# Kernel tuning notes

Hardware: AMD Instinct MI355X
Metric: run time of the kernel (lower is better)

## Reference

```python
import jax, jax.numpy as jnp
import numpy as np

N_STEPS = 8          # spatial_interval
SPATIAL_SCALE = 1.0  # spatial_scale


def setup_inputs() -> dict:
    key = jax.random.key(0)
    ks = jax.random.split(key, 6)
    B, N, D = 32, 1024, 256
    x = jax.random.normal(ks[0], (B, N, D), dtype=jnp.float32)
    adj_mx = jax.random.uniform(ks[1], (N, N), dtype=jnp.float32) / N  # row-scaled dense adjacency
    alpha_train = jnp.ones((N,), dtype=jnp.float32)          # alpha * ones(num_node), alpha=1.0
    w = jnp.eye(D, dtype=jnp.float32) + 0.01 * jax.random.normal(ks[2], (D, D), dtype=jnp.float32)
    d = jax.random.uniform(ks[3], (D,), dtype=jnp.float32)
    fc_in_w = jax.random.normal(ks[4], (D, D), dtype=jnp.float32) * (1.0 / np.sqrt(D))
    fc_in_b = jnp.zeros((D,), dtype=jnp.float32)
    return {"x": x, "adj_mx": adj_mx, "alpha_train": alpha_train, "w": w,
            "d": d, "fc_in_w": fc_in_w, "fc_in_b": fc_in_b, "vt": 0}


def reference(x, adj_mx, alpha_train, w, d, fc_in_w, fc_in_b, vt):
    # x: [B, N, D]. x0 is detached in torch (x.clone().detach()).
    x0 = jax.lax.stop_gradient(x)
    # fc_in (dropout is identity in eval mode)
    h = jnp.einsum('bnd,ed->bne', x, fc_in_w) + fc_in_b
    # constants of the diffusion ODE
    alph = jax.nn.sigmoid(alpha_train)[:, None]          # [N, 1]
    d_clamped = jnp.clip(d, 0.0, 1.0)
    w_eff = (w * d_clamped) @ w.T                        # [D, D]
    dt = jnp.float32(SPATIAL_SCALE / N_STEPS)

    def euler_step(h, _):
        ax = jnp.einsum('nm,bmd->bnd', adj_mx, h)        # graph diffusion
        f = alph * 0.5 * (ax - h) + h @ w_eff - h + x0
        return h + dt * f, None

    h, _ = jax.lax.scan(euler_step, h, None, length=N_STEPS)
    return h
```

## Files before the change

### kernel.cpp

```cpp
#include <hip/hip_runtime.h>
#include <hip/hip_bf16.h>
#include <stdint.h>

typedef __bf16 bf16;
typedef __bf16 bf16x8 __attribute__((ext_vector_type(8)));
typedef __bf16 bf16x4 __attribute__((ext_vector_type(4)));
typedef float f32x4 __attribute__((ext_vector_type(4)));
typedef unsigned short u16;

__device__ __forceinline__ void gload_lds16(const bf16* g, bf16* l) {
    __builtin_amdgcn_global_load_lds(
        (const __attribute__((address_space(1))) void*)g,
        (__attribute__((address_space(3))) void*)l, 16, 0, 0);
}

template <int LD>
__device__ __forceinline__ void stage(const bf16* __restrict__ g, bf16* l, int t) {
    int sw = ((t & 7) ^ ((t >> 3) & 7)) << 3;
    size_t base = (size_t)(t >> 3) * LD + sw;
#pragma unroll
    for (int k = 0; k < 4; ++k)
        gload_lds16(g + base + (size_t)(k * 32) * LD, l + t * 8 + k * 2048);
}

#define LDSW(buf, row, kc) \
    (*(const bf16x8*)&(buf)[(row) * 64 + ((((kc) ^ ((row) & 7))) << 3)])

__global__ void prep_alpha(const float* __restrict__ a, float* __restrict__ out) {
    int i = blockIdx.x * blockDim.x + threadIdx.x;
    if (i < 1024) out[i] = 0.5f / (1.0f + __expf(-a[i]));
}

__global__ void prep_adj(const float* __restrict__ adj, const float* __restrict__ ahs,
                         bf16* __restrict__ adjb) {
    int i = blockIdx.x * blockDim.x + threadIdx.x;
    int row = i >> 8;
    float s = ahs[row];
    float4 v = ((const float4*)adj)[i];
    bf16x4 o = {(bf16)(s * v.x), (bf16)(s * v.y), (bf16)(s * v.z), (bf16)(s * v.w)};
    ((bf16x4*)adjb)[i] = o;
}

__global__ void cast_f32_bf16x4(const float* __restrict__ src, bf16* __restrict__ dst,
                                int n4) {
    int i = blockIdx.x * blockDim.x + threadIdx.x;
    if (i < n4) {
        float4 v = ((const float4*)src)[i];
        bf16x4 o = {(bf16)v.x, (bf16)v.y, (bf16)v.z, (bf16)v.w};
        ((bf16x4*)dst)[i] = o;
    }
}

__global__ void prep_weff(const float* __restrict__ w, const float* __restrict__ dv,
                          bf16* __restrict__ weffT) {
    __shared__ float wk[256];
    __shared__ float dd[256];
    int k = blockIdx.x, j = threadIdx.x;
    dd[j] = fminf(fmaxf(dv[j], 0.0f), 1.0f);
    wk[j] = w[k * 256 + j];
    __syncthreads();
    float s = 0.0f;
#pragma unroll 8
    for (int c = 0; c < 256; ++c) s += wk[c] * dd[c] * w[j * 256 + c];
    weffT[j * 256 + k] = (bf16)s;
}

__global__ void prep_xT(const float* __restrict__ x, bf16* __restrict__ xT,
                        bf16* __restrict__ xb) {
    __shared__ bf16 tile[64][65];
    int b = blockIdx.z, n0 = blockIdx.x * 64, d0 = blockIdx.y * 64;
    int t = threadIdx.x;
    int i = t >> 4, j4 = (t & 15) * 4;
#pragma unroll
    for (int p = 0; p < 4; ++p) {
        int n = i + p * 16;
        size_t gi = (((size_t)b << 10) + n0 + n) * 256 + d0 + j4;
        float4 v = *(const float4*)&x[gi];
        bf16x4 o = {(bf16)v.x, (bf16)v.y, (bf16)v.z, (bf16)v.w};
        *(bf16x4*)&xb[gi] = o;
        tile[n][j4 + 0] = o[0]; tile[n][j4 + 1] = o[1];
        tile[n][j4 + 2] = o[2]; tile[n][j4 + 3] = o[3];
    }
    __syncthreads();
#pragma unroll
    for (int p = 0; p < 4; ++p) {
        int c = p * 256 + t;
        int d = c >> 4, nc = c & 15;
        bf16x4 o = {tile[nc * 4 + 0][d], tile[nc * 4 + 1][d],
                    tile[nc * 4 + 2][d], tile[nc * 4 + 3][d]};
        *(bf16x4*)&xT[(((size_t)(b * 256 + d0 + d)) << 10) + n0 + nc * 4] = o;
    }
}

__device__ __forceinline__ void stChunk(const bf16* __restrict__ g, int ld,
                                        bf16* l, int c) {
    int row = c >> 3, slot = c & 7;
    gload_lds16(g + (size_t)row * ld + ((slot ^ (row & 7)) << 3), l + c * 8);
}
__device__ __forceinline__ void stageA4(const bf16* __restrict__ g, int lda,
                                        bf16* l, int t) {
#pragma unroll
    for (int i = 0; i < 4; ++i) stChunk(g, lda, l, (i << 8) + t);
}
__device__ __forceinline__ void stageB2(const bf16* __restrict__ g, int ldb,
                                        bf16* l, int t) {
#pragma unroll
    for (int i = 0; i < 2; ++i) stChunk(g, ldb, l, (i << 8) + t);
}

__device__ __forceinline__ void mma_tile(const bf16* A, const bf16* B,
                                         f32x4 acc[2][4], int lane, int wv) {
    const int r0 = wv * 32 + (lane & 15);
    const int kq = lane >> 4;
    bf16x8 a[2][2], b[4][2];
#pragma unroll
    for (int mi = 0; mi < 2; ++mi) {
        int rA = r0 + mi * 16;
#pragma unroll
        for (int kk = 0; kk < 2; ++kk) a[mi][kk] = LDSW(A, rA, kk * 4 + kq);
    }
#pragma unroll
    for (int ni = 0; ni < 4; ++ni) {
        int rB = ni * 16 + (lane & 15);
#pragma unroll
        for (int kk = 0; kk < 2; ++kk) b[ni][kk] = LDSW(B, rB, kk * 4 + kq);
    }
#pragma unroll
    for (int kk = 0; kk < 2; ++kk)
#pragma unroll
        for (int mi = 0; mi < 2; ++mi)
#pragma unroll
            for (int ni = 0; ni < 4; ++ni)
                acc[mi][ni] = __builtin_amdgcn_mfma_f32_16x16x32_bf16(
                    a[mi][kk], b[ni][kk], acc[mi][ni], 0, 0, 0);
}

template <int NT, typename F>
__device__ __forceinline__ void run_pipeline(F tadr, bf16 (*As)[8192],
                                             bf16 (*Bs)[4096], f32x4 acc[2][4],
                                             int t, int lane, int wv) {
    {
        const bf16 *Ag, *Bg; int lda, ldb;
        tadr(0, Ag, lda, Bg, ldb);
        stageA4(Ag, lda, As[0], t);
        stageB2(Bg, ldb, Bs[0], t);
        if (NT > 1) {
            tadr(1, Ag, lda, Bg, ldb);
            stageA4(Ag, lda, As[1], t);
            stageB2(Bg, ldb, Bs[1], t);
        }
    }
    int cur = 0, pre = 2;
#pragma unroll 1
    for (int i = 0; i < NT; ++i) {
        if (i + 2 < NT) {
            const bf16 *Ag, *Bg; int lda, ldb;
            tadr(i + 2, Ag, lda, Bg, ldb);
            stageA4(Ag, lda, As[pre], t);
            stageB2(Bg, ldb, Bs[pre], t);
            asm volatile("s_waitcnt vmcnt(12)" ::: "memory");
        } else if (i + 1 < NT) {
            asm volatile("s_waitcnt vmcnt(6)" ::: "memory");
        } else {
            asm volatile("s_waitcnt vmcnt(0)" ::: "memory");
        }
        __builtin_amdgcn_s_barrier();
        mma_tile(As[cur], Bs[cur], acc, lane, wv);
        __builtin_amdgcn_s_barrier();
        cur = (cur == 2) ? 0 : cur + 1;
        pre = (pre == 2) ? 0 : pre + 1;
    }
}

__launch_bounds__(256, 2)
__global__ void gemm_fcin(const bf16* __restrict__ xb, const bf16* __restrict__ fcwb,
                          const float* __restrict__ fcb,
                          bf16* __restrict__ hb, bf16* __restrict__ hT,
                          bf16* __restrict__ hloT) {
    __shared__ __align__(16) bf16 As[3][8192];
    __shared__ __align__(16) bf16 Bs[3][4096];
    int t = threadIdx.x, lane = t & 63, wv = t >> 6;
    int row0 = blockIdx.y * 128;
    int col0 = blockIdx.x * 64;
    f32x4 acc[2][4] = {};
    const bf16* Ab = xb + (size_t)row0 * 256;
    const bf16* Bb = fcwb + (size_t)col0 * 256;
    auto tadr = [&](int i, const bf16*& Ag, int& lda, const bf16*& Bg, int& ldb) {
        Ag = Ab + i * 64; lda = 256;
        Bg = Bb + i * 64; ldb = 256;
    };
    run_pipeline<4>(tadr, As, Bs, acc, t, lane, wv);

    int rbase = row0 + wv * 32 + ((lane >> 4) << 2);
    int cbase = col0 + (lane & 15);
#pragma unroll
    for (int mi = 0; mi < 2; ++mi) {
        int rg = rbase + mi * 16;
#pragma unroll
        for (int ni = 0; ni < 4; ++ni) {
            int col = cbase + ni * 16;
            float bias = fcb[col];
            bf16x4 tv, lv;
#pragma unroll
            for (int r = 0; r < 4; ++r) {
                float v = acc[mi][ni][r] + bias;
                size_t idx = (size_t)(rg + r) * 256 + col;
                bf16 hi = (bf16)v;
                hb[idx] = hi;
                tv[r] = hi;
                lv[r] = (bf16)(v - (float)hi);
            }
            int b = rg >> 10, n = rg & 1023;
            size_t tb = (((size_t)(b * 256 + col)) << 10) + n;
            *(bf16x4*)&hT[tb] = tv;
            *(bf16x4*)&hloT[tb] = lv;
        }
    }
}

template <bool LAST>
__launch_bounds__(256, 2)
__global__ void gemm_step(const bf16* __restrict__ adjb, const bf16* __restrict__ hbp,
                          const bf16* __restrict__ hTp, const bf16* __restrict__ weffT,
                          const float* __restrict__ ahs, const bf16* __restrict__ xT,
                          bf16* __restrict__ hloT, bf16* __restrict__ hbn,
                          bf16* __restrict__ hTn, float* __restrict__ out) {
    __shared__ __align__(16) char smem[65536];
    bf16 (*As)[8192] = (bf16(*)[8192])smem;
    bf16 (*Bs)[8192] = (bf16(*)[8192])(smem + 32768);
    int t = threadIdx.x, lane = t & 63, wv = t >> 6;
    int wm = wv >> 1, wn = wv & 1;
    int g = blockIdx.x;
    int xcd = g & 7, rest = g >> 3;
    int b = (rest & 3) * 8 + xcd;
    int tile = rest >> 2;
    int n0 = (tile & 7) * 128;
    int d0 = (tile >> 3) * 128;
    f32x4 acc[4][4] = {};

    const bf16* A1 = adjb + (size_t)n0 * 1024;
    const bf16* B1 = hTp + ((size_t)(b * 256 + d0)) * 1024;
    const bf16* A2 = hbp + ((size_t)(b * 1024 + n0)) * 256;
    const bf16* B2 = weffT + (size_t)d0 * 256;

    const int l15 = lane & 15, kq = lane >> 4;
    int rA[4], rB[4];
#pragma unroll
    for (int j = 0; j < 4; ++j) {
        rA[j] = wm * 64 + j * 16 + l15;
        rB[j] = wn * 64 + j * 16 + l15;
    }

    stage<1024>(A1, As[0], t);
    stage<1024>(B1, Bs[0], t);

#pragma unroll 1
    for (int i = 0; i < 20; ++i) {
        if (i + 1 < 20) {
            if (i + 1 < 16) {
                stage<1024>(A1 + (i + 1) * 64, As[(i + 1) & 1], t);
                stage<1024>(B1 + (i + 1) * 64, Bs[(i + 1) & 1], t);
            } else {
                stage<256>(A2 + (i - 15) * 64, As[(i + 1) & 1], t);
                stage<256>(B2 + (i - 15) * 64, Bs[(i + 1) & 1], t);
            }
            asm volatile("s_waitcnt vmcnt(8)" ::: "memory");
        } else {
            asm volatile("s_waitcnt vmcnt(0)" ::: "memory");
        }
        __builtin_amdgcn_s_barrier();
        const bf16* A = As[i & 1];
        const bf16* B = Bs[i & 1];
#pragma unroll
        for (int kk = 0; kk < 2; ++kk) {
            int kc = kk * 4 + kq;
            bf16x8 a[4], bfr[4];
#pragma unroll
            for (int j = 0; j < 4; ++j) bfr[j] = LDSW(B, rB[j], kc);
#pragma unroll
            for (int j = 0; j < 4; ++j) a[j] = LDSW(A, rA[j], kc);
#pragma unroll
            for (int mi = 0; mi < 4; ++mi)
#pragma unroll
                for (int ni = 0; ni < 4; ++ni)
                    acc[mi][ni] = __builtin_amdgcn_mfma_f32_16x16x32_bf16(
                        a[mi], bfr[ni], acc[mi][ni], 0, 0, 0);
        }
        __builtin_amdgcn_s_barrier();
    }

    const float dt = 0.125f;
    const int lq = (lane >> 4) << 2;
    bf16* img = (bf16*)smem;
    const int PADN = 132;
#pragma unroll
    for (int mi = 0; mi < 4; ++mi) {
        int nl = wm * 64 + mi * 16 + lq;
        int ng = n0 + nl;
        f32x4 av = *(const f32x4*)&ahs[ng];
#pragma unroll
        for (int ni = 0; ni < 4; ++ni) {
            int cl = wn * 64 + ni * 16 + l15;
            int cg = d0 + cl;
            size_t tb = (((size_t)(b * 256 + cg)) << 10) + ng;
            bf16x4 hp = *(const bf16x4*)&hTp[tb];
            bf16x4 lp = *(const bf16x4*)&hloT[tb];
            bf16x4 xp = *(const bf16x4*)&xT[tb];
            bf16x4 nhi, nlo;
#pragma unroll
            for (int r = 0; r < 4; ++r) {
                float hold = (float)hp[r] + (float)lp[r];
                float f = acc[mi][ni][r] - (av[r] + 1.0f) * hold + (float)xp[r];
                float hv = hold + dt * f;
                if (LAST) {
                    out[(((size_t)b << 10) + ng + r) * 256 + cg] = hv;
                } else {
                    bf16 hi2 = (bf16)hv;
                    nhi[r] = hi2;
                    nlo[r] = (bf16)(hv - (float)hi2);
                }
            }
            if (!LAST) {
                *(bf16x4*)&hTn[tb] = nhi;
                *(bf16x4*)&hloT[tb] = nlo;
                int nsw = nl ^ (((cl >> 3) & 7) << 2);
                *(bf16x4*)&img[cl * PADN + nsw] = nhi;
            }
        }
    }
    if (!LAST) {
        asm volatile("s_waitcnt lgkmcnt(0)" ::: "memory");
        __builtin_amdgcn_s_barrier();
        const u16* imgu = (const u16*)img;
#pragma unroll
        for (int P = 0; P < 8; ++P) {
            int chunk = P * 256 + t;
            int node = chunk >> 4;
            int c8 = chunk & 15;
            u16 v[8];
#pragma unroll
            for (int k = 0; k < 8; ++k) {
                int col = c8 * 8 + k;
                v[k] = imgu[col * PADN + (node ^ (((col >> 3) & 7) << 2))];
            }
            uint4 pk;
            pk.x = v[0] | ((unsigned)v[1] << 16);
            pk.y = v[2] | ((unsigned)v[3] << 16);
            pk.z = v[4] | ((unsigned)v[5] << 16);
            pk.w = v[6] | ((unsigned)v[7] << 16);
            *(uint4*)&hbn[(((size_t)b << 10) + n0 + node) * 256 + d0 + c8 * 8] = pk;
        }
    }
}

extern "C" void kernel_launch(void* const* d_in, const int* in_sizes, int n_in,
                              void* d_out, int out_size, void* d_ws, size_t ws_size,
                              hipStream_t stream) {
    const float* x     = (const float*)d_in[0];
    const float* adj   = (const float*)d_in[1];
    const float* alpha = (const float*)d_in[2];
    const float* w     = (const float*)d_in[3];
    const float* dvec  = (const float*)d_in[4];
    const float* fcw   = (const float*)d_in[5];
    const float* fcb   = (const float*)d_in[6];
    float* out = (float*)d_out;

    const size_t HB = (size_t)32 * 1024 * 256 * 2;
    char* p = (char*)d_ws;
    bf16* hb0   = (bf16*)p; p += HB;
    bf16* hb1   = (bf16*)p; p += HB;
    bf16* hT0   = (bf16*)p; p += HB;
    bf16* hT1   = (bf16*)p; p += HB;
    bf16* xb    = (bf16*)p; p += HB;
    bf16* hloT  = (bf16*)p; p += HB;
    bf16* xT    = (bf16*)p; p += HB;
    bf16* adjb  = (bf16*)p; p += (size_t)1024 * 1024 * 2;
    bf16* fcwb  = (bf16*)p; p += 256 * 256 * 2;
    bf16* weffT = (bf16*)p; p += 256 * 256 * 2;
    float* ahs  = (float*)p; p += 1024 * 4;

    prep_alpha<<<4, 256, 0, stream>>>(alpha, ahs);
    prep_adj<<<1024, 256, 0, stream>>>(adj, ahs, adjb);
    prep_weff<<<256, 256, 0, stream>>>(w, dvec, weffT);
    prep_xT<<<dim3(16, 4, 32), 256, 0, stream>>>(x, xT, xb);
    cast_f32_bf16x4<<<64, 256, 0, stream>>>(fcw, fcwb, 16384);

    gemm_fcin<<<dim3(4, 256), 256, 0, stream>>>(xb, fcwb, fcb, hb0, hT0, hloT);

    bf16* hb[2] = {hb0, hb1};
    bf16* hT[2] = {hT0, hT1};
    int cur = 0;
    for (int s = 0; s < 8; ++s) {
        if (s < 7)
            gemm_step<false><<<512, 256, 0, stream>>>(
                adjb, hb[cur], hT[cur], weffT, ahs, xT, hloT,
                hb[cur ^ 1], hT[cur ^ 1], out);
        else
            gemm_step<true><<<512, 256, 0, stream>>>(
                adjb, hb[cur], hT[cur], weffT, ahs, xT, hloT,
                hb[cur ^ 1], hT[cur ^ 1], out);
        cur ^= 1;
    }
}
```

Before: 378.3 us.

## Load GEMM operands directly from global into registers, bypassing LDS staging

Replaces the double-buffered global-to-LDS staging with barriers in gemm_step. Each wave now loads its own MFMA fragments straight from global memory into registers, ping-ponging between two register sets so the next k-block's loads overlap the current MFMAs. This removes the LDS round trip and the block-wide barriers, and cuts shared memory to the epilogue image, which may allow more resident blocks. The cost is that tiles shared between waves are fetched redundantly from global/L2, and the loads are strided per row and less coalesced, with higher register pressure.

```diff
diff --git a/kernel.cpp b/kernel.cpp
--- a/kernel.cpp
+++ b/kernel.cpp
@@ -13,18 +13,6 @@
         (const __attribute__((address_space(1))) void*)g,
         (__attribute__((address_space(3))) void*)l, 16, 0, 0);
 }
-
-template <int LD>
-__device__ __forceinline__ void stage(const bf16* __restrict__ g, bf16* l, int t) {
-    int sw = ((t & 7) ^ ((t >> 3) & 7)) << 3;
-    size_t base = (size_t)(t >> 3) * LD + sw;
-#pragma unroll
-    for (int k = 0; k < 4; ++k)
-        gload_lds16(g + base + (size_t)(k * 32) * LD, l + t * 8 + k * 2048);
-}
-
-#define LDSW(buf, row, kc) \
-    (*(const bf16x8*)&(buf)[(row) * 64 + ((((kc) ^ ((row) & 7))) << 3)])
 
 __global__ void prep_alpha(const float* __restrict__ a, float* __restrict__ out) {
     int i = blockIdx.x * blockDim.x + threadIdx.x;
@@ -107,6 +95,9 @@
 #pragma unroll
     for (int i = 0; i < 2; ++i) stChunk(g, ldb, l, (i << 8) + t);
 }
+
+#define LDSW(buf, row, kc) \
+    (*(const bf16x8*)&(buf)[(row) * 64 + ((((kc) ^ ((row) & 7))) << 3)])
 
 __device__ __forceinline__ void mma_tile(const bf16* A, const bf16* B,
                                          f32x4 acc[2][4], int lane, int wv) {
@@ -225,9 +216,7 @@
                           const float* __restrict__ ahs, const bf16* __restrict__ xT,
                           bf16* __restrict__ hloT, bf16* __restrict__ hbn,
                           bf16* __restrict__ hTn, float* __restrict__ out) {
-    __shared__ __align__(16) char smem[65536];
-    bf16 (*As)[8192] = (bf16(*)[8192])smem;
-    bf16 (*Bs)[8192] = (bf16(*)[8192])(smem + 32768);
+    __shared__ __align__(16) bf16 img[128 * 132];
     int t = threadIdx.x, lane = t & 63, wv = t >> 6;
     int wm = wv >> 1, wn = wv & 1;
     int g = blockIdx.x;
@@ -243,7 +232,8 @@
     const bf16* A2 = hbp + ((size_t)(b * 1024 + n0)) * 256;
     const bf16* B2 = weffT + (size_t)d0 * 256;
 
-    const int l15 = lane & 15, kq = lane >> 4;
+    const int l15 = lane & 15;
+    const int ko = (lane >> 4) << 3;
     int rA[4], rB[4];
 #pragma unroll
     for (int j = 0; j < 4; ++j) {
@@ -251,47 +241,41 @@
         rB[j] = wn * 64 + j * 16 + l15;
     }
 
-    stage<1024>(A1, As[0], t);
-    stage<1024>(B1, Bs[0], t);
-
-#pragma unroll 1
-    for (int i = 0; i < 20; ++i) {
-        if (i + 1 < 20) {
-            if (i + 1 < 16) {
-                stage<1024>(A1 + (i + 1) * 64, As[(i + 1) & 1], t);
-                stage<1024>(B1 + (i + 1) * 64, Bs[(i + 1) & 1], t);
-            } else {
-                stage<256>(A2 + (i - 15) * 64, As[(i + 1) & 1], t);
-                stage<256>(B2 + (i - 15) * 64, Bs[(i + 1) & 1], t);
-            }
-            asm volatile("s_waitcnt vmcnt(8)" ::: "memory");
-        } else {
-            asm volatile("s_waitcnt vmcnt(0)" ::: "memory");
-        }
-        __builtin_amdgcn_s_barrier();
-        const bf16* A = As[i & 1];
-        const bf16* B = Bs[i & 1];
-#pragma unroll
-        for (int kk = 0; kk < 2; ++kk) {
-            int kc = kk * 4 + kq;
-            bf16x8 a[4], bfr[4];
-#pragma unroll
-            for (int j = 0; j < 4; ++j) bfr[j] = LDSW(B, rB[j], kc);
-#pragma unroll
-            for (int j = 0; j < 4; ++j) a[j] = LDSW(A, rA[j], kc);
+    auto LD = [&](int i, bf16x8 (&af)[4][2], bf16x8 (&bg)[4][2]) {
+        const bf16 *PA, *PB; int la, lb, off;
+        if (i < 16) { PA = A1; la = 1024; PB = B1; lb = 1024; off = i * 64; }
+        else        { PA = A2; la = 256;  PB = B2; lb = 256;  off = (i - 16) * 64; }
+#pragma unroll
+        for (int j = 0; j < 4; ++j)
+#pragma unroll
+            for (int kk = 0; kk < 2; ++kk) {
+                af[j][kk] = *(const bf16x8*)&PA[(size_t)rA[j] * la + off + kk * 32 + ko];
+                bg[j][kk] = *(const bf16x8*)&PB[(size_t)rB[j] * lb + off + kk * 32 + ko];
+            }
+    };
+    auto MMA = [&](bf16x8 (&af)[4][2], bf16x8 (&bg)[4][2]) {
+#pragma unroll
+        for (int kk = 0; kk < 2; ++kk)
 #pragma unroll
             for (int mi = 0; mi < 4; ++mi)
 #pragma unroll
                 for (int ni = 0; ni < 4; ++ni)
                     acc[mi][ni] = __builtin_amdgcn_mfma_f32_16x16x32_bf16(
-                        a[mi], bfr[ni], acc[mi][ni], 0, 0, 0);
-        }
-        __builtin_amdgcn_s_barrier();
+                        af[mi][kk], bg[ni][kk], acc[mi][ni], 0, 0, 0);
+    };
+
+    bf16x8 aE[4][2], bE[4][2], aO[4][2], bO[4][2];
+    LD(0, aE, bE);
+#pragma unroll 1
+    for (int i = 0; i < 20; i += 2) {
+        LD(i + 1, aO, bO);
+        MMA(aE, bE);
+        if (i + 2 < 20) LD(i + 2, aE, bE);
+        MMA(aO, bO);
     }
 
     const float dt = 0.125f;
     const int lq = (lane >> 4) << 2;
-    bf16* img = (bf16*)smem;
     const int PADN = 132;
 #pragma unroll
     for (int mi = 0; mi < 4; ++mi) {
```

Result: slower. 777.8 us (+105.6%).
